# Kernel optimization log

Hardware: AMD Instinct MI355X
Metric: run time of the kernel (lower is better)

The kernel has to match this reference:

```python
import jax, jax.numpy as jnp
import numpy as np

# Static config matching init_kwargs
V, D, BW, GS = 128000, 1024, 4, 256
G = D // GS                  # n_groups = 4
PACK = 8 // BW               # 2 indices per byte
PD = D // PACK               # packed_dim = 512
N_LEVELS = 2 ** BW           # 16
ROT_SEED = 42
SCALE = float(np.sqrt(GS))   # self._scale


def _group_signs():
    # Deterministic Rademacher sign flips per group (seed = rotation_seed + g_start),
    # the random part of the randomized-Hadamard inverse rotation.
    s = np.stack([
        np.random.RandomState(ROT_SEED + g * GS).choice(
            np.array([-1.0, 1.0], dtype=np.float32), size=GS)
        for g in range(G)
    ])
    return jnp.asarray(s)  # [G, GS]

SIGNS = _group_signs()


def fwht(x):
    """Fast Walsh-Hadamard transform along last axis (power-of-2 length)."""
    d = x.shape[-1]
    lead = x.shape[:-1]
    x = x.reshape(-1, d)
    h = 1
    while h < d:  # fixed log2(d) iterations (static)
        x = x.reshape(-1, d // (2 * h), 2, h)
        a, b = x[:, :, 0, :], x[:, :, 1, :]
        x = jnp.stack([a + b, a - b], axis=2).reshape(-1, d)
        h *= 2
    return x.reshape(*lead, d)


def setup_inputs() -> dict:
    key = jax.random.key(0)
    k1, k2, k3, k4 = jax.random.split(key, 4)
    return {
        "input_ids": jax.random.randint(k1, (8, 4096), 0, V, dtype=jnp.int32),
        "indices_packed": jax.random.randint(k2, (V, PD), 0, 256, dtype=jnp.int32),
        "weight_norms": jax.random.uniform(k3, (V, G), dtype=jnp.float32),
        "codebook": jax.random.normal(k4, (N_LEVELS,), dtype=jnp.float32),
    }


def reference(input_ids, indices_packed, weight_norms, codebook):
    orig_shape = input_ids.shape
    flat_ids = input_ids.reshape(-1)                      # [N]
    packed = indices_packed[flat_ids]                     # [N, PD] (byte values)
    # Unpack 4-bit indices, little-endian within each byte
    pos = jnp.arange(D)
    byte = packed[:, pos // PACK]                         # [N, D]
    shift = (pos % PACK) * BW
    idx = (byte >> shift) & (N_LEVELS - 1)                # [N, D] in [0, 16)
    # Codebook lookup + scale
    Y = codebook[idx] / SCALE                             # [N, D]
    Yg = Y.reshape(-1, G, GS)                             # [N, G, GS]
    # Inverse randomized Hadamard rotation: normalized FWHT then sign flips
    Wg = fwht(Yg) * (SIGNS / jnp.sqrt(jnp.float32(GS)))   # [N, G, GS]
    # Per-row, per-group norm rescale
    Wg = Wg * weight_norms[flat_ids][:, :, None]
    return Wg.reshape(*orig_shape, D)
```

## Files before the change

kernel.cpp:

```cpp
#include <hip/hip_runtime.h>


#define NGROUP 4
#define GSIZE  256

struct SignBits { unsigned w[NGROUP][GSIZE / 32]; };

constexpr SignBits gen_sign_bits() {
    SignBits S{};
    for (int g = 0; g < NGROUP; ++g) {
        unsigned mt[624] = {};
        unsigned s = 42u + (unsigned)g * 256u;
        for (int i = 0; i < 624; ++i) {
            mt[i] = s;
            s = 1812433253u * (s ^ (s >> 30)) + (unsigned)(i + 1);
        }
        for (int i = 0; i < 624; ++i) {
            unsigned y = (mt[i] & 0x80000000u) | (mt[(i + 1) % 624] & 0x7fffffffu);
            mt[i] = mt[(i + 397) % 624] ^ (y >> 1) ^ ((y & 1u) ? 0x9908b0dfu : 0u);
        }
        for (int e = 0; e < GSIZE; ++e) {
            unsigned y = mt[e];
            y ^= y >> 11;
            y ^= (y << 7) & 0x9d2c5680u;
            y ^= (y << 15) & 0xefc60000u;
            y ^= y >> 18;
            if (y & 1u) S.w[g][e >> 5] |= (1u << (e & 31));
        }
    }
    return S;
}

__constant__ SignBits c_sign = gen_sign_bits();

__global__ __launch_bounds__(256) void turboquant_kernel(
    const int*   __restrict__ input_ids,
    const int*   __restrict__ indices_packed,
    const float* __restrict__ weight_norms,
    const float* __restrict__ codebook,
    float*       __restrict__ out)
{
    const int token = blockIdx.x;
    const int tid   = threadIdx.x;
    const int g     = tid >> 6;
    const int l     = tid & 63;

    const int id = input_ids[token];

    const float cbv = codebook[l & 15];

    const int2 pw = *(const int2*)(indices_packed + (size_t)id * 512 + g * 128 + 2 * l);

    const int n0 =  pw.x        & 15;
    const int n1 = (pw.x >> 4)  & 15;
    const int n2 =  pw.y        & 15;
    const int n3 = (pw.y >> 4)  & 15;

    float y0 = __shfl(cbv, n0);
    float y1 = __shfl(cbv, n1);
    float y2 = __shfl(cbv, n2);
    float y3 = __shfl(cbv, n3);

    float a, b;
    a = y0 + y1; b = y0 - y1; y0 = a; y1 = b;
    a = y2 + y3; b = y2 - y3; y2 = a; y3 = b;
    a = y0 + y2; b = y0 - y2; y0 = a; y2 = b;
    a = y1 + y3; b = y1 - y3; y1 = a; y3 = b;
#pragma unroll
    for (int m = 1; m <= 32; m <<= 1) {
        const float o0 = __shfl_xor(y0, m);
        const float o1 = __shfl_xor(y1, m);
        const float o2 = __shfl_xor(y2, m);
        const float o3 = __shfl_xor(y3, m);
        const bool up = (l & m) != 0;
        y0 = up ? (o0 - y0) : (y0 + o0);
        y1 = up ? (o1 - y1) : (y1 + o1);
        y2 = up ? (o2 - y2) : (y2 + o2);
        y3 = up ? (o3 - y3) : (y3 + o3);
    }

    const float norm  = weight_norms[(size_t)id * 4 + g];
    const float scale = norm * (1.0f / 256.0f);

    const unsigned w = c_sign.w[g][l >> 3];
    const int bb = (l & 7) * 4;
    const float s0 = ((w >> (bb + 0)) & 1u) ? scale : -scale;
    const float s1 = ((w >> (bb + 1)) & 1u) ? scale : -scale;
    const float s2 = ((w >> (bb + 2)) & 1u) ? scale : -scale;
    const float s3 = ((w >> (bb + 3)) & 1u) ? scale : -scale;

    float4 o;
    o.x = y0 * s0;
    o.y = y1 * s1;
    o.z = y2 * s2;
    o.w = y3 * s3;
    ((float4*)out)[(size_t)token * 256 + g * 64 + l] = o;
}

extern "C" void kernel_launch(void* const* d_in, const int* in_sizes, int n_in,
                              void* d_out, int out_size, void* d_ws, size_t ws_size,
                              hipStream_t stream) {
    const int*   input_ids      = (const int*)d_in[0];
    const int*   indices_packed = (const int*)d_in[1];
    const float* weight_norms   = (const float*)d_in[2];
    const float* codebook       = (const float*)d_in[3];
    float*       out            = (float*)d_out;

    const int n_tokens = in_sizes[0];

    turboquant_kernel<<<n_tokens, 256, 0, stream>>>(
        input_ids, indices_packed, weight_norms, codebook, out);
}
```

Baseline: 365.0 us.

## Process four tokens per block with pair-LUT decode and fewer FWHT shuffles

New measurement: 357.0 us. 2.2% less time.

```diff
diff --git a/kernel.cpp b/kernel.cpp
--- a/kernel.cpp
+++ b/kernel.cpp
@@ -2,12 +2,11 @@
 
 
 #define NGROUP 4
-#define GSIZE  256
 
-struct SignBits { unsigned w[NGROUP][GSIZE / 32]; };
+struct SignTbl { unsigned short u[NGROUP][16]; };
 
-constexpr SignBits gen_sign_bits() {
-    SignBits S{};
+constexpr SignTbl gen_sign_tbl() {
+    SignTbl T{};
     for (int g = 0; g < NGROUP; ++g) {
         unsigned mt[624] = {};
         unsigned s = 42u + (unsigned)g * 256u;
@@ -19,82 +18,102 @@
             unsigned y = (mt[i] & 0x80000000u) | (mt[(i + 1) % 624] & 0x7fffffffu);
             mt[i] = mt[(i + 397) % 624] ^ (y >> 1) ^ ((y & 1u) ? 0x9908b0dfu : 0u);
         }
-        for (int e = 0; e < GSIZE; ++e) {
+        unsigned neg[256] = {};
+        for (int e = 0; e < 256; ++e) {
             unsigned y = mt[e];
             y ^= y >> 11;
             y ^= (y << 7) & 0x9d2c5680u;
             y ^= (y << 15) & 0xefc60000u;
             y ^= y >> 18;
-            if (y & 1u) S.w[g][e >> 5] |= (1u << (e & 31));
+            neg[e] = (y & 1u) ? 0u : 1u;
         }
+        for (int i = 0; i < 16; ++i)
+            for (int m = 0; m < 4; ++m)
+                for (int k = 0; k < 4; ++k)
+                    if (neg[4 * i + 64 * m + k])
+                        T.u[g][i] |= (unsigned short)(1u << (4 * m + k));
     }
-    return S;
+    return T;
 }
 
-__constant__ SignBits c_sign = gen_sign_bits();
+__constant__ SignTbl c_sign = gen_sign_tbl();
 
 __global__ __launch_bounds__(256) void turboquant_kernel(
     const int*   __restrict__ input_ids,
     const int*   __restrict__ indices_packed,
     const float* __restrict__ weight_norms,
     const float* __restrict__ codebook,
-    float*       __restrict__ out)
+    float*       __restrict__ out,
+    int n_tokens)
 {
-    const int token = blockIdx.x;
-    const int tid   = threadIdx.x;
-    const int g     = tid >> 6;
-    const int l     = tid & 63;
+    __shared__ float2 lut[256];
+    const int tid = threadIdx.x;
+    {
+        const float lo = codebook[tid & 15];
+        const float hi = codebook[tid >> 4];
+        lut[tid] = make_float2(lo + hi, lo - hi);
+    }
+    __syncthreads();
+
+    const int token = blockIdx.x * 4 + (tid >> 6);
+    if (token >= n_tokens) return;
+
+    const int l = tid & 63;
+    const int g = l >> 4;
+    const int i = l & 15;
 
     const int id = input_ids[token];
+    const int* row = indices_packed + (size_t)id * 512 + g * 128 + 2 * i;
 
-    const float cbv = codebook[l & 15];
-
-    const int2 pw = *(const int2*)(indices_packed + (size_t)id * 512 + g * 128 + 2 * l);
-
-    const int n0 =  pw.x        & 15;
-    const int n1 = (pw.x >> 4)  & 15;
-    const int n2 =  pw.y        & 15;
-    const int n3 = (pw.y >> 4)  & 15;
-
-    float y0 = __shfl(cbv, n0);
-    float y1 = __shfl(cbv, n1);
-    float y2 = __shfl(cbv, n2);
-    float y3 = __shfl(cbv, n3);
-
-    float a, b;
-    a = y0 + y1; b = y0 - y1; y0 = a; y1 = b;
-    a = y2 + y3; b = y2 - y3; y2 = a; y3 = b;
-    a = y0 + y2; b = y0 - y2; y0 = a; y2 = b;
-    a = y1 + y3; b = y1 - y3; y1 = a; y3 = b;
+    float v[4][4];
 #pragma unroll
-    for (int m = 1; m <= 32; m <<= 1) {
-        const float o0 = __shfl_xor(y0, m);
-        const float o1 = __shfl_xor(y1, m);
-        const float o2 = __shfl_xor(y2, m);
-        const float o3 = __shfl_xor(y3, m);
-        const bool up = (l & m) != 0;
-        y0 = up ? (o0 - y0) : (y0 + o0);
-        y1 = up ? (o1 - y1) : (y1 + o1);
-        y2 = up ? (o2 - y2) : (y2 + o2);
-        y3 = up ? (o3 - y3) : (y3 + o3);
+    for (int m = 0; m < 4; ++m) {
+        const int2 w = *(const int2*)(row + 32 * m);
+        const float2 p0 = lut[w.x & 255];
+        const float2 p1 = lut[w.y & 255];
+        v[m][0] = p0.x + p1.x;
+        v[m][2] = p0.x - p1.x;
+        v[m][1] = p0.y + p1.y;
+        v[m][3] = p0.y - p1.y;
     }
 
-    const float norm  = weight_norms[(size_t)id * 4 + g];
-    const float scale = norm * (1.0f / 256.0f);
+#pragma unroll
+    for (int mask = 1; mask <= 8; mask <<= 1) {
+        const unsigned sm = (i & mask) ? 0x80000000u : 0u;
+#pragma unroll
+        for (int m = 0; m < 4; ++m) {
+#pragma unroll
+            for (int k = 0; k < 4; ++k) {
+                const float o = __shfl_xor(v[m][k], mask);
+                v[m][k] = o + __uint_as_float(__float_as_uint(v[m][k]) ^ sm);
+            }
+        }
+    }
 
-    const unsigned w = c_sign.w[g][l >> 3];
-    const int bb = (l & 7) * 4;
-    const float s0 = ((w >> (bb + 0)) & 1u) ? scale : -scale;
-    const float s1 = ((w >> (bb + 1)) & 1u) ? scale : -scale;
-    const float s2 = ((w >> (bb + 2)) & 1u) ? scale : -scale;
-    const float s3 = ((w >> (bb + 3)) & 1u) ? scale : -scale;
+#pragma unroll
+    for (int k = 0; k < 4; ++k) {
+        const float a = v[0][k], b = v[1][k], c = v[2][k], d = v[3][k];
+        const float ab0 = a + b, ab1 = a - b, cd0 = c + d, cd1 = c - d;
+        v[0][k] = ab0 + cd0;
+        v[2][k] = ab0 - cd0;
+        v[1][k] = ab1 + cd1;
+        v[3][k] = ab1 - cd1;
+    }
 
-    float4 o;
-    o.x = y0 * s0;
-    o.y = y1 * s1;
-    o.z = y2 * s2;
-    o.w = y3 * s3;
-    ((float4*)out)[(size_t)token * 256 + g * 64 + l] = o;
+    const float    norm       = weight_norms[(size_t)id * 4 + g];
+    const unsigned scale_bits = __float_as_uint(norm * (1.0f / 256.0f));
+    const unsigned u          = (unsigned)c_sign.u[g][i];
+
+    float* obase = out + (size_t)token * 1024 + g * 256 + 4 * i;
+#pragma unroll
+    for (int m = 0; m < 4; ++m) {
+        float4 o;
+        o.x = v[m][0] * __uint_as_float(((u << (31 - (4 * m + 0))) & 0x80000000u) ^ scale_bits);
+        o.y = v[m][1] * __uint_as_float(((u << (31 - (4 * m + 1))) & 0x80000000u) ^ scale_bits);
+        o.z = v[m][2] * __uint_as_float(((u << (31 - (4 * m + 2))) & 0x80000000u) ^ scale_bits);
+        o.w = v[m][3] * __uint_as_float(((u << (31 - (4 * m + 3))) & 0x80000000u) ^ scale_bits);
+        *(float4*)(obase + 64 * m) = o;
+    }
 }
 
 extern "C" void kernel_launch(void* const* d_in, const int* in_sizes, int n_in,
@@ -108,6 +127,6 @@
 
     const int n_tokens = in_sizes[0];
 
-    turboquant_kernel<<<n_tokens, 256, 0, stream>>>(
-        input_ids, indices_packed, weight_norms, codebook, out);
+    turboquant_kernel<<<(n_tokens + 3) / 4, 256, 0, stream>>>(
+        input_ids, indices_packed, weight_norms, codebook, out, n_tokens);
 }
```
